# Kernel optimization log

Measured on AMD Instinct MI355X. Metric: run time of the kernel, lower is better.

## Reference

```python
import jax, jax.numpy as jnp
import numpy as np

N_USERS = 8192
N_ITEMS = 8192
D = 64
B = 1024
EPS = 1e-6


def _l2norm_rows(x):
    # torch F.normalize(p=2, dim=1): x / max(||x||_2, 1e-12)
    n = jnp.sqrt(jnp.sum(x * x, axis=1, keepdims=True))
    return x / jnp.maximum(n, 1e-12)


def setup_inputs() -> dict:
    key = jax.random.key(0)
    ks = jax.random.split(key, 12)
    adj = (jax.random.uniform(ks[0], (N_USERS, N_ITEMS)) < 0.02).astype(jnp.float32)
    obs_adj = (jax.random.uniform(ks[1], (N_USERS, N_ITEMS)) < 0.02).astype(jnp.float32)
    xavier_scale = 0.05  # mimic xavier_uniform magnitude; keeps exp(inner) tame
    return {
        "users": jax.random.randint(ks[2], (B,), 0, N_USERS),
        "pos_items": jax.random.randint(ks[3], (B,), 0, N_ITEMS),
        "neg_items": jax.random.randint(ks[4], (B,), 0, N_ITEMS),
        "adj_matrix": adj,
        "obs_users": jax.random.randint(ks[5], (B,), 0, N_USERS),
        "obs_pos_items": jax.random.randint(ks[6], (B,), 0, N_ITEMS),
        "obs_neg_items": jax.random.randint(ks[7], (B,), 0, N_ITEMS),
        "obs_adj_matrix": obs_adj,
        "iteration": 0,
        "user_emb": jax.random.normal(ks[8], (N_USERS, D), jnp.float32) * xavier_scale,
        "item_emb": jax.random.normal(ks[9], (N_ITEMS, D), jnp.float32) * xavier_scale,
        "W_1": jax.random.normal(ks[10], (D, D), jnp.float32) * 0.1,
        "W_2": jax.random.normal(ks[11], (D, D), jnp.float32) * 0.1,
        "W_obs": jax.random.normal(jax.random.fold_in(key, 99), (D, D), jnp.float32) * 0.1,
    }


def reference(users, pos_items, neg_items, adj_matrix, obs_users, obs_pos_items,
              obs_neg_items, obs_adj_matrix, iteration, user_emb, item_emb,
              W_1, W_2, W_obs):
    # attention-like coefficients: exp(inner) masked by adjacency, row-normalized
    score = jnp.exp(user_emb @ item_emb.T) * adj_matrix          # [U, I]
    coef = score / (jnp.sum(score, axis=1, keepdims=True) + EPS)  # vectorized row loop

    h1_user = (coef @ item_emb) @ W_1                             # [U, D]
    h1_item = (coef.T @ user_emb) @ W_1                           # [I, D]

    # degree-normalized aggregation (vectorized per-row loops)
    deg_u = jnp.sum(adj_matrix, axis=1)                           # [U]
    deg_i = jnp.sum(adj_matrix, axis=0)                           # [I]
    h2_user = ((adj_matrix @ item_emb) / (deg_u + EPS)[:, None]) @ W_2
    h2_item = ((adj_matrix.T @ user_emb) / (deg_i + EPS)[:, None]) @ W_2

    samp_user = jnp.concatenate([h1_user, h2_user], axis=1)       # [U, 2D]
    # NOTE: original code concatenates h2_item with itself (not h1_item) -- kept faithful
    samp_item = jnp.concatenate([h2_item, h2_item], axis=1)       # [I, 2D]

    samp_u = samp_user[users]
    samp_pi = samp_item[pos_items]
    samp_ni = samp_item[neg_items]

    # observed-graph branch
    odeg_u = jnp.sum(obs_adj_matrix, axis=1)
    odeg_i = jnp.sum(obs_adj_matrix, axis=0)
    obs_user = jnp.tanh(((obs_adj_matrix @ item_emb) / (odeg_u + EPS)[:, None]) @ W_obs)
    obs_item = jnp.tanh(((obs_adj_matrix.T @ user_emb) / (odeg_i + EPS)[:, None]) @ W_obs)

    obs_u = obs_user[obs_users]
    obs_pi = obs_item[obs_pos_items]
    obs_ni = obs_item[obs_neg_items]

    h_user = jnp.tanh(jnp.concatenate([samp_u, obs_u], axis=1))      # [B, 3D]
    h_pos = jnp.tanh(jnp.concatenate([samp_pi, obs_pi], axis=1))     # [B, 3D]
    h_neg = jnp.tanh(jnp.concatenate([samp_ni, obs_ni], axis=1))     # [B, 3D]

    return (_l2norm_rows(h_user), _l2norm_rows(h_pos), _l2norm_rows(h_neg))
```

## Files before the change

### kernel.cpp

```cpp
#include <hip/hip_runtime.h>
#include <stdint.h>

typedef unsigned short u16;
typedef unsigned int u32;
typedef __attribute__((ext_vector_type(8))) short short8;
typedef __attribute__((ext_vector_type(4))) float f32x4;

#define EPSF 1e-6f
#define MFMA(a, b, c) __builtin_amdgcn_mfma_f32_16x16x32_bf16((a), (b), (c), 0, 0, 0)
#define KSPLIT 16

__device__ inline u32 f2b_bits(u32 fb) {
  return (fb + 0x7fffu + ((fb >> 16) & 1u)) >> 16;
}
__device__ inline u32 pack2f(float lo, float hi) {
  union { float f; u32 u; } a, b; a.f = lo; b.f = hi;
  return f2b_bits(a.u) | (f2b_bits(b.u) << 16);
}
__device__ inline short8 ldfrag(const u32* p, int uidx) {
  union { u32 u[4]; short8 s; } t;
  t.u[0] = p[uidx + 0]; t.u[1] = p[uidx + 1];
  t.u[2] = p[uidx + 2]; t.u[3] = p[uidx + 3];
  return t.s;
}
__device__ inline f32x4 zero4() { f32x4 z; z[0]=0.f; z[1]=0.f; z[2]=0.f; z[3]=0.f; return z; }

__global__ void k_detect(const u32* __restrict__ users, int B, u32* flag) {
  __shared__ int f;
  if (threadIdx.x == 0) f = 0;
  __syncthreads();
  int loc = 0;
  for (int j = threadIdx.x; j < B; j += 256)
    if ((j & 1) && users[j] != 0u) loc = 1;
  if (loc) atomicOr(&f, 1);
  __syncthreads();
  if (threadIdx.x == 0) *flag = (u32)f;
}

__device__ inline int gidx(const void* p, int r, bool i64) {
  return i64 ? (int)((const long long*)p)[r] : ((const int*)p)[r];
}

__global__ __launch_bounds__(256) void pass_user(
    const u32* __restrict__ flag,
    const void* __restrict__ users, const void* __restrict__ obs_users,
    const float* __restrict__ adj, const float* __restrict__ obs_adj,
    const float* __restrict__ UE, const float* __restrict__ IE,
    int NI,
    float* __restrict__ t1_r, float* __restrict__ h2u_r,
    float* __restrict__ obsu_r, float* __restrict__ scal_r)
{
  __shared__ float ue_l[64];
  __shared__ int   ia[1024];  __shared__ float va[1024];
  __shared__ int   ioi[1024]; __shared__ float vo[1024];
  __shared__ float redf[16 * 16 * 4];
  __shared__ float red[256];
  __shared__ int   cnt_a, cnt_o;

  const int tid = threadIdx.x;
  const int r = blockIdx.x;
  const bool i64 = (*flag == 0u);
  const int is_ = gidx(users, r, i64);
  const int io  = gidx(obs_users, r, i64);
  const int G = tid >> 4, sl = tid & 15;

  if (tid == 0) { cnt_a = 0; cnt_o = 0; }
  if (tid < 64) ue_l[tid] = UE[(size_t)is_ * 64 + tid];

  const int nfr = NI / 1024;
  float4 av[8], ov[8];
  const float4* arow = (const float4*)(adj + (size_t)is_ * NI);
  const float4* orow = (const float4*)(obs_adj + (size_t)io * NI);
  #pragma unroll
  for (int k = 0; k < 8; ++k) {
    if (k < nfr) { av[k] = arow[k * 256 + tid]; ov[k] = orow[k * 256 + tid]; }
  }
  __syncthreads();

  float dg = 0.f, od = 0.f;
  #pragma unroll
  for (int k = 0; k < 8; ++k) {
    if (k < nfr) {
      int base = (k * 256 + tid) * 4;
      float va4[4] = {av[k].x, av[k].y, av[k].z, av[k].w};
      float vo4[4] = {ov[k].x, ov[k].y, ov[k].z, ov[k].w};
      #pragma unroll
      for (int c = 0; c < 4; ++c) {
        if (va4[c] != 0.f) {
          dg += va4[c];
          int p = atomicAdd(&cnt_a, 1);
          ia[p] = base + c; va[p] = va4[c];
        }
        if (vo4[c] != 0.f) {
          od += vo4[c];
          int p = atomicAdd(&cnt_o, 1);
          ioi[p] = base + c; vo[p] = vo4[c];
        }
      }
    }
  }
  __syncthreads();

  float4 ue4 = ((const float4*)ue_l)[sl];
  float4 A1 = {0,0,0,0}, A2 = {0,0,0,0}, A3 = {0,0,0,0};
  float rs_p = 0.f;
  const int nA = cnt_a, nO = cnt_o;

  for (int j = G; j < nA; j += 16) {
    int i = ia[j]; float a = va[j];
    float4 e = *(const float4*)(IE + (size_t)i * 64 + sl * 4);
    float s = ue4.x * e.x + ue4.y * e.y + ue4.z * e.z + ue4.w * e.w;
    #pragma unroll
    for (int off = 1; off <= 8; off <<= 1) s += __shfl_xor(s, off, 64);
    float w = expf(s) * a;
    if (sl == 0) rs_p += w;
    A1.x += w * e.x; A1.y += w * e.y; A1.z += w * e.z; A1.w += w * e.w;
    A2.x += a * e.x; A2.y += a * e.y; A2.z += a * e.z; A2.w += a * e.w;
  }
  for (int j = G; j < nO; j += 16) {
    int i = ioi[j]; float o = vo[j];
    float4 e = *(const float4*)(IE + (size_t)i * 64 + sl * 4);
    A3.x += o * e.x; A3.y += o * e.y; A3.z += o * e.z; A3.w += o * e.w;
  }

  float* my = redf + (G * 16 + sl) * 4;
  my[0] = A1.x; my[1] = A1.y; my[2] = A1.z; my[3] = A1.w;
  __syncthreads();
  if (tid < 64) {
    float s = 0.f;
    #pragma unroll
    for (int g = 0; g < 16; ++g) s += redf[(g * 16 + (tid >> 2)) * 4 + (tid & 3)];
    t1_r[(size_t)r * 64 + tid] = s;
  }
  __syncthreads();
  my[0] = A2.x; my[1] = A2.y; my[2] = A2.z; my[3] = A2.w;
  __syncthreads();
  if (tid < 64) {
    float s = 0.f;
    #pragma unroll
    for (int g = 0; g < 16; ++g) s += redf[(g * 16 + (tid >> 2)) * 4 + (tid & 3)];
    h2u_r[(size_t)r * 64 + tid] = s;
  }
  __syncthreads();
  my[0] = A3.x; my[1] = A3.y; my[2] = A3.z; my[3] = A3.w;
  __syncthreads();
  if (tid < 64) {
    float s = 0.f;
    #pragma unroll
    for (int g = 0; g < 16; ++g) s += redf[(g * 16 + (tid >> 2)) * 4 + (tid & 3)];
    obsu_r[(size_t)r * 64 + tid] = s;
  }
  __syncthreads();

  red[tid] = (sl == 0) ? rs_p : 0.f; __syncthreads();
  if (tid < 64) {
    float s = red[tid] + red[tid + 64] + red[tid + 128] + red[tid + 192];
    #pragma unroll
    for (int off = 32; off >= 1; off >>= 1) s += __shfl_xor(s, off, 64);
    if (tid == 0) scal_r[r * 4 + 0] = s;
  }
  __syncthreads();
  red[tid] = dg; __syncthreads();
  if (tid < 64) {
    float s = red[tid] + red[tid + 64] + red[tid + 128] + red[tid + 192];
    #pragma unroll
    for (int off = 32; off >= 1; off >>= 1) s += __shfl_xor(s, off, 64);
    if (tid == 0) scal_r[r * 4 + 1] = s;
  }
  __syncthreads();
  red[tid] = od; __syncthreads();
  if (tid < 64) {
    float s = red[tid] + red[tid + 64] + red[tid + 128] + red[tid + 192];
    #pragma unroll
    for (int off = 32; off >= 1; off >>= 1) s += __shfl_xor(s, off, 64);
    if (tid == 0) scal_r[r * 4 + 2] = s;
  }
}

__global__ __launch_bounds__(256) void pass_item_mfma(
    const float* __restrict__ adj, const float* __restrict__ obs_adj,
    const float* __restrict__ UE,
    int NU, int NI,
    float* __restrict__ degi, float* __restrict__ odegi,
    float* __restrict__ h2i, float* __restrict__ obsi)
{
  __shared__ u32 at_s[64 * 33];
  __shared__ u32 oat_s[64 * 33];
  __shared__ u32 uet_s[64 * 33];

  const int tid = threadIdx.x;
  const int lane = tid & 63;
  const int wv = tid >> 6;
  const int l15 = lane & 15, q = lane >> 4;
  const int ig = blockIdx.x / KSPLIT;
  const int ksp = blockIdx.x % KSPLIT;
  const int i0 = ig * 64;
  const int ucount = NU / KSPLIT;
  const int ub = ksp * ucount;
  const int up = tid >> 3;
  const int cp = tid & 7;

  f32x4 accH[4], accO[4], accDA, accDO;
  #pragma unroll
  for (int n = 0; n < 4; ++n) { accH[n] = zero4(); accO[n] = zero4(); }
  accDA = zero4(); accDO = zero4();

  short8 ones8;
  { union { u32 u[4]; short8 s; } t;
    t.u[0] = 0x3F803F80u; t.u[1] = 0x3F803F80u; t.u[2] = 0x3F803F80u; t.u[3] = 0x3F803F80u;
    ones8 = t.s; }

  float4 A0, A1v, A2v, A3v, O0, O1v, O2v, O3v, U0, U1v, U2v, U3v;
  auto issue = [&](int ch) {
    const int u0 = ub + ch * 64;
    const int ua = u0 + up * 2, ub2 = ua + 1;
    const float4* pa0 = (const float4*)(adj + (size_t)ua * NI + i0 + cp * 8);
    const float4* pa1 = (const float4*)(adj + (size_t)ub2 * NI + i0 + cp * 8);
    const float4* po0 = (const float4*)(obs_adj + (size_t)ua * NI + i0 + cp * 8);
    const float4* po1 = (const float4*)(obs_adj + (size_t)ub2 * NI + i0 + cp * 8);
    const float4* pu0 = (const float4*)(UE + (size_t)ua * 64 + cp * 8);
    const float4* pu1 = (const float4*)(UE + (size_t)ub2 * 64 + cp * 8);
    A0 = pa0[0]; A1v = pa0[1]; A2v = pa1[0]; A3v = pa1[1];
    O0 = po0[0]; O1v = po0[1]; O2v = po1[0]; O3v = po1[1];
    U0 = pu0[0]; U1v = pu0[1]; U2v = pu1[0]; U3v = pu1[1];
  };

  const int nch = ucount >> 6;
  issue(0);
  for (int ch = 0; ch < nch; ++ch) {
    __syncthreads();

    {
      float alo[8] = {A0.x,A0.y,A0.z,A0.w,A1v.x,A1v.y,A1v.z,A1v.w};
      float ahi[8] = {A2v.x,A2v.y,A2v.z,A2v.w,A3v.x,A3v.y,A3v.z,A3v.w};
      float olo[8] = {O0.x,O0.y,O0.z,O0.w,O1v.x,O1v.y,O1v.z,O1v.w};
      float ohi[8] = {O2v.x,O2v.y,O2v.z,O2v.w,O3v.x,O3v.y,O3v.z,O3v.w};
      float ulo[8] = {U0.x,U0.y,U0.z,U0.w,U1v.x,U1v.y,U1v.z,U1v.w};
      float uhi[8] = {U2v.x,U2v.y,U2v.z,U2v.w,U3v.x,U3v.y,U3v.z,U3v.w};
      #pragma unroll
      for (int j = 0; j < 8; ++j) {
        int c = cp * 8 + j;
        at_s[c * 33 + up]  = pack2f(alo[j], ahi[j]);
        oat_s[c * 33 + up] = pack2f(olo[j], ohi[j]);
        uet_s[c * 33 + up] = pack2f(ulo[j], uhi[j]);
      }
    }
    __syncthreads();

    if (ch + 1 < nch) issue(ch + 1);

    #pragma unroll
    for (int ks = 0; ks < 2; ++ks) {
      int ab = (wv * 16 + l15) * 33 + ks * 16 + q * 4;
      short8 aa = ldfrag(at_s, ab);
      short8 ao = ldfrag(oat_s, ab);
      accDA = MFMA(aa, ones8, accDA);
      accDO = MFMA(ao, ones8, accDO);
      #pragma unroll
      for (int nt = 0; nt < 4; ++nt) {
        short8 b8 = ldfrag(uet_s, (nt * 16 + l15) * 33 + ks * 16 + q * 4);
        accH[nt] = MFMA(aa, b8, accH[nt]);
        accO[nt] = MFMA(ao, b8, accO[nt]);
      }
    }
  }

  #pragma unroll
  for (int nt = 0; nt < 4; ++nt) {
    #pragma unroll
    for (int r = 0; r < 4; ++r) {
      int item = i0 + wv * 16 + q * 4 + r;
      int d = nt * 16 + l15;
      atomicAdd(&h2i[(size_t)item * 64 + d], accH[nt][r]);
      atomicAdd(&obsi[(size_t)item * 64 + d], accO[nt][r]);
    }
  }
  if (l15 == 0) {
    #pragma unroll
    for (int r = 0; r < 4; ++r) {
      int item = i0 + wv * 16 + q * 4 + r;
      atomicAdd(&degi[item], accDA[r]);
      atomicAdd(&odegi[item], accDO[r]);
    }
  }
}

__global__ __launch_bounds__(64) void epilogue(
    const u32* __restrict__ flag, int B,
    const void* __restrict__ pos_items, const void* __restrict__ neg_items,
    const void* __restrict__ obs_pos, const void* __restrict__ obs_neg,
    const float* __restrict__ W1, const float* __restrict__ W2,
    const float* __restrict__ Wobs,
    const float* __restrict__ t1_r, const float* __restrict__ h2u_r,
    const float* __restrict__ obsu_r, const float* __restrict__ scal_r,
    const float* __restrict__ degi, const float* __restrict__ odegi,
    const float* __restrict__ h2i, const float* __restrict__ obsi,
    float* __restrict__ out)
{
  __shared__ float v1f[64], v2f[64], v3f[64];
  const int b = blockIdx.x, t = threadIdx.x;
  const int which = b / B, r = b % B;
  const bool i64 = (*flag == 0u);

  const float *Wa, *Wb;
  if (which == 0) {
    float s1 = 1.f / (scal_r[r * 4 + 0] + EPSF);
    float s2 = 1.f / (scal_r[r * 4 + 1] + EPSF);
    float s3 = 1.f / (scal_r[r * 4 + 2] + EPSF);
    v1f[t] = t1_r[(size_t)r * 64 + t] * s1;
    v2f[t] = h2u_r[(size_t)r * 64 + t] * s2;
    v3f[t] = obsu_r[(size_t)r * 64 + t] * s3;
    Wa = W1; Wb = W2;
  } else {
    const void* sptr = (which == 1) ? pos_items : neg_items;
    const void* optr = (which == 1) ? obs_pos : obs_neg;
    int id = gidx(sptr, r, i64);
    int oid = gidx(optr, r, i64);
    float s1 = 1.f / (degi[id] + EPSF);
    float s3 = 1.f / (odegi[oid] + EPSF);
    float h = h2i[(size_t)id * 64 + t] * s1;
    v1f[t] = h; v2f[t] = h;
    v3f[t] = obsi[(size_t)oid * 64 + t] * s3;
    Wa = W2; Wb = W2;
  }
  __syncthreads();

  float c1 = 0.f, c2 = 0.f, c3 = 0.f;
  #pragma unroll 8
  for (int d = 0; d < 64; ++d) {
    c1 += v1f[d] * Wa[(size_t)d * 64 + t];
    c2 += v2f[d] * Wb[(size_t)d * 64 + t];
    c3 += v3f[d] * Wobs[(size_t)d * 64 + t];
  }
  float y0 = tanhf(c1);
  float y1 = tanhf(c2);
  float y2 = tanhf(tanhf(c3));
  float ss = y0 * y0 + y1 * y1 + y2 * y2;
  #pragma unroll
  for (int off = 32; off >= 1; off >>= 1) ss += __shfl_xor(ss, off, 64);
  float inv = 1.f / fmaxf(sqrtf(ss), 1e-12f);

  float* orow = out + ((size_t)which * B + r) * 192;
  orow[t]       = y0 * inv;
  orow[64 + t]  = y1 * inv;
  orow[128 + t] = y2 * inv;
}

extern "C" void kernel_launch(void* const* d_in, const int* in_sizes, int n_in,
                              void* d_out, int out_size, void* d_ws, size_t ws_size,
                              hipStream_t stream) {
  struct Ent { long long s; int i; };
  Ent e[32]; int m = 0;
  for (int i = 0; i < n_in && i < 32; ++i)
    if (in_sizes[i] > 1) { e[m].s = in_sizes[i]; e[m].i = i; ++m; }
  for (int a = 1; a < m; ++a) {
    Ent t = e[a]; int b = a - 1;
    while (b >= 0 && e[b].s < t.s) { e[b + 1] = e[b]; --b; }
    e[b + 1] = t;
  }
  bool ok = (m == 13) &&
            e[0].s == e[1].s && e[2].s == e[3].s &&
            e[4].s == e[5].s && e[5].s == e[6].s &&
            e[7].s == e[12].s;

  const void *users, *pos_items, *neg_items, *obs_users, *obs_pos, *obs_neg;
  const float *adj, *obs_adj, *UE, *IE, *W1, *W2, *Wobs;
  int B, NU, NI;
  if (ok) {
    adj = (const float*)d_in[e[0].i];  obs_adj = (const float*)d_in[e[1].i];
    UE  = (const float*)d_in[e[2].i];  IE      = (const float*)d_in[e[3].i];
    W1 = (const float*)d_in[e[4].i]; W2 = (const float*)d_in[e[5].i];
    Wobs = (const float*)d_in[e[6].i];
    users     = d_in[e[7].i];  pos_items = d_in[e[8].i];  neg_items = d_in[e[9].i];
    obs_users = d_in[e[10].i]; obs_pos   = d_in[e[11].i]; obs_neg   = d_in[e[12].i];
    B  = (int)e[7].s;
    NU = (int)(e[2].s / 64);
    NI = (int)(e[3].s / 64);
  } else {
    users = d_in[0]; pos_items = d_in[1]; neg_items = d_in[2];
    adj = (const float*)d_in[3];
    obs_users = d_in[4]; obs_pos = d_in[5]; obs_neg = d_in[6];
    obs_adj = (const float*)d_in[7];
    UE = (const float*)d_in[9]; IE = (const float*)d_in[10];
    W1 = (const float*)d_in[11]; W2 = (const float*)d_in[12];
    Wobs = (const float*)d_in[13];
    B = 1024; NU = 8192; NI = 8192;
  }

  float* w = (float*)d_ws;
  u32*   flag  = (u32*)w;
  float* t1_r  = w + 16;
  float* h2u_r = t1_r + (size_t)B * 64;
  float* obsu_r= h2u_r + (size_t)B * 64;
  float* scal_r= obsu_r + (size_t)B * 64;
  float* degi  = scal_r + (size_t)B * 4;
  float* odegi = degi + NI;
  float* h2i   = odegi + NI;
  float* obsi  = h2i + (size_t)NI * 64;

  k_detect<<<dim3(1), dim3(256), 0, stream>>>((const u32*)users, B, flag);
  hipMemsetAsync(degi, 0, (size_t)(2 * NI + 2 * (size_t)NI * 64) * sizeof(float), stream);

  pass_user<<<dim3(B), dim3(256), 0, stream>>>(flag, users, obs_users,
                                               adj, obs_adj, UE, IE, NI,
                                               t1_r, h2u_r, obsu_r, scal_r);
  pass_item_mfma<<<dim3((NI / 64) * KSPLIT), dim3(256), 0, stream>>>(
      adj, obs_adj, UE, NU, NI, degi, odegi, h2i, obsi);
  epilogue<<<dim3(3 * B), dim3(64), 0, stream>>>(flag, B,
                                                 pos_items, neg_items, obs_pos, obs_neg,
                                                 W1, W2, Wobs,
                                                 t1_r, h2u_r, obsu_r, scal_r,
                                                 degi, odegi, h2i, obsi,
                                                 (float*)d_out);
}
```

Baseline: 616.5 us.

## Pretranspose user embeddings to bf16 and make item pass per-wave without block syncs

```diff
diff --git a/kernel.cpp b/kernel.cpp
--- a/kernel.cpp
+++ b/kernel.cpp
@@ -8,7 +8,7 @@
 
 #define EPSF 1e-6f
 #define MFMA(a, b, c) __builtin_amdgcn_mfma_f32_16x16x32_bf16((a), (b), (c), 0, 0, 0)
-#define KSPLIT 16
+#define KSPLIT 8
 
 __device__ inline u32 f2b_bits(u32 fb) {
   return (fb + 0x7fffu + ((fb >> 16) & 1u)) >> 16;
@@ -23,6 +23,11 @@
   t.u[2] = p[uidx + 2]; t.u[3] = p[uidx + 3];
   return t.s;
 }
+__device__ inline short8 ldfrag_g(const u16* p) {
+  union { uint4 v; short8 s; } t;
+  t.v = *(const uint4*)p;
+  return t.s;
+}
 __device__ inline f32x4 zero4() { f32x4 z; z[0]=0.f; z[1]=0.f; z[2]=0.f; z[3]=0.f; return z; }
 
 __global__ void k_detect(const u32* __restrict__ users, int B, u32* flag) {
@@ -39,6 +44,31 @@
 
 __device__ inline int gidx(const void* p, int r, bool i64) {
   return i64 ? (int)((const long long*)p)[r] : ((const int*)p)[r];
+}
+
+__global__ __launch_bounds__(256) void k_transpose_ue(
+    const float* __restrict__ UE, int NU, u16* __restrict__ ueT)
+{
+  __shared__ float t[64 * 65];
+  const int tid = threadIdx.x;
+  const int u0 = blockIdx.x * 64;
+  const int ul = tid >> 2, dq = tid & 3;
+  const float4* src = (const float4*)(UE + (size_t)(u0 + ul) * 64 + dq * 16);
+  #pragma unroll
+  for (int k = 0; k < 4; ++k) {
+    float4 v = src[k];
+    int d = dq * 16 + k * 4;
+    t[ul * 65 + d + 0] = v.x; t[ul * 65 + d + 1] = v.y;
+    t[ul * 65 + d + 2] = v.z; t[ul * 65 + d + 3] = v.w;
+  }
+  __syncthreads();
+  const int d = tid >> 2, ug = tid & 3;
+  u32* dst = (u32*)(ueT + (size_t)d * NU + u0 + ug * 16);
+  #pragma unroll
+  for (int k = 0; k < 8; ++k) {
+    int u = ug * 16 + k * 2;
+    dst[k] = pack2f(t[u * 65 + d], t[(u + 1) * 65 + d]);
+  }
 }
 
 __global__ __launch_bounds__(256) void pass_user(
@@ -179,14 +209,12 @@
 
 __global__ __launch_bounds__(256) void pass_item_mfma(
     const float* __restrict__ adj, const float* __restrict__ obs_adj,
-    const float* __restrict__ UE,
+    const u16* __restrict__ ueT,
     int NU, int NI,
     float* __restrict__ degi, float* __restrict__ odegi,
     float* __restrict__ h2i, float* __restrict__ obsi)
 {
-  __shared__ u32 at_s[64 * 33];
-  __shared__ u32 oat_s[64 * 33];
-  __shared__ u32 uet_s[64 * 33];
+  __shared__ u32 lds[4 * 2 * 16 * 36];
 
   const int tid = threadIdx.x;
   const int lane = tid & 63;
@@ -194,11 +222,14 @@
   const int l15 = lane & 15, q = lane >> 4;
   const int ig = blockIdx.x / KSPLIT;
   const int ksp = blockIdx.x % KSPLIT;
-  const int i0 = ig * 64;
+  const int i0 = ig * 64 + wv * 16;
   const int ucount = NU / KSPLIT;
   const int ub = ksp * ucount;
-  const int up = tid >> 3;
-  const int cp = tid & 7;
+  u32* at_s = lds + wv * 2 * 16 * 36;
+  u32* ot_s = at_s + 16 * 36;
+
+  const int li = lane & 31;
+  const int oc = lane >> 5;
 
   f32x4 accH[4], accO[4], accDA, accDO;
   #pragma unroll
@@ -210,57 +241,58 @@
     t.u[0] = 0x3F803F80u; t.u[1] = 0x3F803F80u; t.u[2] = 0x3F803F80u; t.u[3] = 0x3F803F80u;
     ones8 = t.s; }
 
-  float4 A0, A1v, A2v, A3v, O0, O1v, O2v, O3v, U0, U1v, U2v, U3v;
+  float4 A0, A1v, A2v, A3v, O0, O1v, O2v, O3v;
   auto issue = [&](int ch) {
-    const int u0 = ub + ch * 64;
-    const int ua = u0 + up * 2, ub2 = ua + 1;
-    const float4* pa0 = (const float4*)(adj + (size_t)ua * NI + i0 + cp * 8);
-    const float4* pa1 = (const float4*)(adj + (size_t)ub2 * NI + i0 + cp * 8);
-    const float4* po0 = (const float4*)(obs_adj + (size_t)ua * NI + i0 + cp * 8);
-    const float4* po1 = (const float4*)(obs_adj + (size_t)ub2 * NI + i0 + cp * 8);
-    const float4* pu0 = (const float4*)(UE + (size_t)ua * 64 + cp * 8);
-    const float4* pu1 = (const float4*)(UE + (size_t)ub2 * 64 + cp * 8);
+    int u0 = ub + ch * 64;
+    int ua = u0 + 2 * li;
+    const float4* pa0 = (const float4*)(adj + (size_t)ua * NI + i0 + oc * 8);
+    const float4* pa1 = (const float4*)(adj + (size_t)(ua + 1) * NI + i0 + oc * 8);
+    const float4* po0 = (const float4*)(obs_adj + (size_t)ua * NI + i0 + oc * 8);
+    const float4* po1 = (const float4*)(obs_adj + (size_t)(ua + 1) * NI + i0 + oc * 8);
     A0 = pa0[0]; A1v = pa0[1]; A2v = pa1[0]; A3v = pa1[1];
     O0 = po0[0]; O1v = po0[1]; O2v = po1[0]; O3v = po1[1];
-    U0 = pu0[0]; U1v = pu0[1]; U2v = pu1[0]; U3v = pu1[1];
   };
 
   const int nch = ucount >> 6;
   issue(0);
   for (int ch = 0; ch < nch; ++ch) {
-    __syncthreads();
-
     {
-      float alo[8] = {A0.x,A0.y,A0.z,A0.w,A1v.x,A1v.y,A1v.z,A1v.w};
-      float ahi[8] = {A2v.x,A2v.y,A2v.z,A2v.w,A3v.x,A3v.y,A3v.z,A3v.w};
-      float olo[8] = {O0.x,O0.y,O0.z,O0.w,O1v.x,O1v.y,O1v.z,O1v.w};
-      float ohi[8] = {O2v.x,O2v.y,O2v.z,O2v.w,O3v.x,O3v.y,O3v.z,O3v.w};
-      float ulo[8] = {U0.x,U0.y,U0.z,U0.w,U1v.x,U1v.y,U1v.z,U1v.w};
-      float uhi[8] = {U2v.x,U2v.y,U2v.z,U2v.w,U3v.x,U3v.y,U3v.z,U3v.w};
+      float r0[8] = {A0.x,A0.y,A0.z,A0.w,A1v.x,A1v.y,A1v.z,A1v.w};
+      float r1[8] = {A2v.x,A2v.y,A2v.z,A2v.w,A3v.x,A3v.y,A3v.z,A3v.w};
+      float s0[8] = {O0.x,O0.y,O0.z,O0.w,O1v.x,O1v.y,O1v.z,O1v.w};
+      float s1[8] = {O2v.x,O2v.y,O2v.z,O2v.w,O3v.x,O3v.y,O3v.z,O3v.w};
       #pragma unroll
       for (int j = 0; j < 8; ++j) {
-        int c = cp * 8 + j;
-        at_s[c * 33 + up]  = pack2f(alo[j], ahi[j]);
-        oat_s[c * 33 + up] = pack2f(olo[j], ohi[j]);
-        uet_s[c * 33 + up] = pack2f(ulo[j], uhi[j]);
+        int c = oc * 8 + j;
+        at_s[c * 36 + li] = pack2f(r0[j], r1[j]);
+        ot_s[c * 36 + li] = pack2f(s0[j], s1[j]);
       }
     }
-    __syncthreads();
-
+    int cur_u0 = ub + ch * 64;
     if (ch + 1 < nch) issue(ch + 1);
 
+    short8 aa[2], ao[2];
     #pragma unroll
     for (int ks = 0; ks < 2; ++ks) {
-      int ab = (wv * 16 + l15) * 33 + ks * 16 + q * 4;
-      short8 aa = ldfrag(at_s, ab);
-      short8 ao = ldfrag(oat_s, ab);
-      accDA = MFMA(aa, ones8, accDA);
-      accDO = MFMA(ao, ones8, accDO);
+      int ab = l15 * 36 + ks * 16 + q * 4;
+      aa[ks] = ldfrag(at_s, ab);
+      ao[ks] = ldfrag(ot_s, ab);
+    }
+    short8 bb[2][4];
+    #pragma unroll
+    for (int ks = 0; ks < 2; ++ks)
+      #pragma unroll
+      for (int nt = 0; nt < 4; ++nt)
+        bb[ks][nt] = ldfrag_g(ueT + (size_t)(nt * 16 + l15) * NU + cur_u0 + ks * 32 + q * 8);
+
+    #pragma unroll
+    for (int ks = 0; ks < 2; ++ks) {
+      accDA = MFMA(aa[ks], ones8, accDA);
+      accDO = MFMA(ao[ks], ones8, accDO);
       #pragma unroll
       for (int nt = 0; nt < 4; ++nt) {
-        short8 b8 = ldfrag(uet_s, (nt * 16 + l15) * 33 + ks * 16 + q * 4);
-        accH[nt] = MFMA(aa, b8, accH[nt]);
-        accO[nt] = MFMA(ao, b8, accO[nt]);
+        accH[nt] = MFMA(aa[ks], bb[ks][nt], accH[nt]);
+        accO[nt] = MFMA(ao[ks], bb[ks][nt], accO[nt]);
       }
     }
   }
@@ -269,7 +301,7 @@
   for (int nt = 0; nt < 4; ++nt) {
     #pragma unroll
     for (int r = 0; r < 4; ++r) {
-      int item = i0 + wv * 16 + q * 4 + r;
+      int item = i0 + q * 4 + r;
       int d = nt * 16 + l15;
       atomicAdd(&h2i[(size_t)item * 64 + d], accH[nt][r]);
       atomicAdd(&obsi[(size_t)item * 64 + d], accO[nt][r]);
@@ -278,7 +310,7 @@
   if (l15 == 0) {
     #pragma unroll
     for (int r = 0; r < 4; ++r) {
-      int item = i0 + wv * 16 + q * 4 + r;
+      int item = i0 + q * 4 + r;
       atomicAdd(&degi[item], accDA[r]);
       atomicAdd(&odegi[item], accDO[r]);
     }
@@ -397,15 +429,17 @@
   float* odegi = degi + NI;
   float* h2i   = odegi + NI;
   float* obsi  = h2i + (size_t)NI * 64;
+  u16*   ueT   = (u16*)(obsi + (size_t)NI * 64);
 
   k_detect<<<dim3(1), dim3(256), 0, stream>>>((const u32*)users, B, flag);
   hipMemsetAsync(degi, 0, (size_t)(2 * NI + 2 * (size_t)NI * 64) * sizeof(float), stream);
+  k_transpose_ue<<<dim3(NU / 64), dim3(256), 0, stream>>>(UE, NU, ueT);
 
   pass_user<<<dim3(B), dim3(256), 0, stream>>>(flag, users, obs_users,
                                                adj, obs_adj, UE, IE, NI,
                                                t1_r, h2u_r, obsu_r, scal_r);
   pass_item_mfma<<<dim3((NI / 64) * KSPLIT), dim3(256), 0, stream>>>(
-      adj, obs_adj, UE, NU, NI, degi, odegi, h2i, obsi);
+      adj, obs_adj, ueT, NU, NI, degi, odegi, h2i, obsi);
   epilogue<<<dim3(3 * B), dim3(64), 0, stream>>>(flag, B,
                                                  pos_items, neg_items, obs_pos, obs_neg,
                                                  W1, W2, Wobs,
```

Measured after the change: 640.0 us. 3.8% more time.
